# Kernel tuning notes

Hardware: AMD Instinct MI355X
Metric: run time of the kernel (lower is better)

## Reference

```python
import jax, jax.numpy as jnp
import numpy as np

B, NV, DM, DK, DV, H, DFF = 256, 40, 512, 256, 256, 4, 2048
K1, K2 = 4, 8
EPS = 1e-5


def _knn_mask(vertices, k):
    # square_distance(xyz, xyz): dist[b,i,j] = ||x_i - x_j||^2
    d = -2.0 * jnp.einsum('bic,bjc->bij', vertices, vertices)
    sq = jnp.sum(vertices ** 2, -1)
    d = d + sq[:, :, None] + sq[:, None, :]
    # torch.topk(dist, k, dim=1, largest=False)[1].transpose(1,2) -> [B,N,k]
    idx = jax.lax.top_k(-jnp.swapaxes(d, 1, 2), k)[1]
    counts = jax.nn.one_hot(idx, NV, dtype=jnp.float32).sum(-2)  # [B,N,NV]
    return (counts < 1.0)[:, None, :, :]  # [B,1,N,N], broadcasts over heads (== repeat)


def _ln(x, g, b):
    m = x.mean(-1, keepdims=True)
    v = x.var(-1, keepdims=True)
    return (x - m) / jnp.sqrt(v + EPS) * g + b


def _encoder(x, mask, wq, bq, wk, bk, wv, bv, wo, bo, ln1g, ln1b, w1, b1, w2, b2, ln2g, ln2b):
    Bn, N, _ = x.shape
    q = (x @ wq + bq).reshape(Bn, N, H, DK).transpose(0, 2, 1, 3)   # [B,H,N,DK]
    kk = (x @ wk + bk).reshape(Bn, N, H, DK).transpose(0, 2, 3, 1)  # [B,H,DK,N]
    v = (x @ wv + bv).reshape(Bn, N, H, DV).transpose(0, 2, 1, 3)   # [B,H,N,DV]
    att = jnp.matmul(q, kk) / np.sqrt(DK)                           # [B,H,N,N]
    att = jnp.where(mask, -jnp.inf, att)
    att = jax.nn.softmax(att, axis=-1)
    o = jnp.matmul(att, v).transpose(0, 2, 1, 3).reshape(Bn, N, H * DV) @ wo + bo
    x = _ln(x + o, ln1g, ln1b)                                      # residual + LayerNorm
    ff = jax.nn.relu(x @ w1 + b1) @ w2 + b2                         # position-wise FFN
    return _ln(x + ff, ln2g, ln2b)


def _fusion(y, w1, b1, bng, bnb, w2, b2):
    y = y @ w1 + b1                       # Conv1d(1024,512,1) == per-position linear
    m = y.mean((0, 1))
    v = y.var((0, 1))                     # BatchNorm1d, training-mode batch stats (biased var)
    y = (y - m) / jnp.sqrt(v + EPS) * bng + bnb
    y = jnp.where(y > 0, y, 0.2 * y)      # LeakyReLU(0.2)
    return y @ w2 + b2                    # Conv1d(512,512,1)


def _forward(vertices, F, *p):
    m1 = _knn_mask(vertices, K1)
    m2 = _knn_mask(vertices, K2)
    F1 = _encoder(F, m1, *p[0:16])
    F2 = _encoder(F, m2, *p[16:32])
    yy = jnp.concatenate((F1, F2), -1)    # [B,N,2*DM]
    return _fusion(yy, *p[32:38])


def setup_inputs() -> dict:
    key = jax.random.key(0)
    d = {}
    cnt = [0]
    def nk():
        cnt[0] += 1
        return jax.random.fold_in(key, cnt[0])
    def lin(i, o):
        return jax.random.normal(nk(), (i, o), jnp.float32) * (1.0 / np.sqrt(i))
    d['vertices'] = jax.random.normal(nk(), (B, NV, 3), jnp.float32)
    d['F'] = jax.random.normal(nk(), (B, NV, DM), jnp.float32)
    for pfx in ('e1', 'e2'):
        d[pfx + '_wq'] = lin(DM, H * DK); d[pfx + '_bq'] = jnp.zeros((H * DK,), jnp.float32)
        d[pfx + '_wk'] = lin(DM, H * DK); d[pfx + '_bk'] = jnp.zeros((H * DK,), jnp.float32)
        d[pfx + '_wv'] = lin(DM, H * DV); d[pfx + '_bv'] = jnp.zeros((H * DV,), jnp.float32)
        d[pfx + '_wo'] = lin(H * DV, DM); d[pfx + '_bo'] = jnp.zeros((DM,), jnp.float32)
        d[pfx + '_ln1g'] = jnp.ones((DM,), jnp.float32); d[pfx + '_ln1b'] = jnp.zeros((DM,), jnp.float32)
        d[pfx + '_w1'] = lin(DM, DFF); d[pfx + '_b1'] = jnp.zeros((DFF,), jnp.float32)
        d[pfx + '_w2'] = lin(DFF, DM); d[pfx + '_b2'] = jnp.zeros((DM,), jnp.float32)
        d[pfx + '_ln2g'] = jnp.ones((DM,), jnp.float32); d[pfx + '_ln2b'] = jnp.zeros((DM,), jnp.float32)
    d['fus_w1'] = lin(2 * DM, DM); d['fus_b1'] = jnp.zeros((DM,), jnp.float32)
    d['fus_bng'] = jnp.ones((DM,), jnp.float32); d['fus_bnb'] = jnp.zeros((DM,), jnp.float32)
    d['fus_w2'] = lin(DM, DM); d['fus_b2'] = jnp.zeros((DM,), jnp.float32)
    return d


def reference(vertices, F,
              e1_wq, e1_bq, e1_wk, e1_bk, e1_wv, e1_bv, e1_wo, e1_bo,
              e1_ln1g, e1_ln1b, e1_w1, e1_b1, e1_w2, e1_b2, e1_ln2g, e1_ln2b,
              e2_wq, e2_bq, e2_wk, e2_bk, e2_wv, e2_bv, e2_wo, e2_bo,
              e2_ln1g, e2_ln1b, e2_w1, e2_b1, e2_w2, e2_b2, e2_ln2g, e2_ln2b,
              fus_w1, fus_b1, fus_bng, fus_bnb, fus_w2, fus_b2):
    return _forward(vertices, F,
                    e1_wq, e1_bq, e1_wk, e1_bk, e1_wv, e1_bv, e1_wo, e1_bo,
                    e1_ln1g, e1_ln1b, e1_w1, e1_b1, e1_w2, e1_b2, e1_ln2g, e1_ln2b,
                    e2_wq, e2_bq, e2_wk, e2_bk, e2_wv, e2_bv, e2_wo, e2_bo,
                    e2_ln1g, e2_ln1b, e2_w1, e2_b1, e2_w2, e2_b2, e2_ln2g, e2_ln2b,
                    fus_w1, fus_b1, fus_bng, fus_bnb, fus_w2, fus_b2)
```

## Files before the change

kernel.cpp:

```cpp
#include <hip/hip_runtime.h>

typedef unsigned short u16;
typedef unsigned int   u32;
typedef __attribute__((ext_vector_type(4))) float f32x4;
typedef __attribute__((ext_vector_type(8))) short short8;
typedef __attribute__((ext_vector_type(4))) unsigned short u16x4;

#define DEV __device__ __forceinline__
#define AS1 __attribute__((address_space(1)))
#define AS3 __attribute__((address_space(3)))
#define SB  __builtin_amdgcn_sched_barrier(0)
#define BAR __builtin_amdgcn_s_barrier()

DEV float bf2f(u16 u){ return __uint_as_float(((u32)u)<<16); }
DEV u16 f2bf(float f){ u32 u=__float_as_uint(f); return (u16)((u + 0x7fffu + ((u>>16)&1u))>>16); }
DEV void g2lds16(const void* g, void* l){
  __builtin_amdgcn_global_load_lds((const AS1 void*)g, (AS3 void*)l, 16, 0, 0);
}

struct WtJobs {
  const float* W[14];
  u16*         WT[14];
  int K[14];
  int N[14];
  int off[15];
};

__global__ __launch_bounds__(256) void wtb_kernel(WtJobs J){
  __shared__ u16 tile[32][33];
  int bid = blockIdx.x;
  int j = 0;
  #pragma unroll
  for (int s=1;s<14;++s) if (bid >= J.off[s]) j = s;
  int lb = bid - J.off[j];
  int K = J.K[j], N = J.N[j];
  int nx = N>>5;
  int n0 = (lb % nx)<<5, k0 = (lb / nx)<<5;
  const float* W = J.W[j];
  u16* WT = J.WT[j];
  int tx = threadIdx.x, ty = threadIdx.y;
  #pragma unroll
  for (int i=0;i<4;++i){
    int k = ty + i*8;
    tile[k][tx] = f2bf(W[(size_t)(k0+k)*N + n0 + tx]);
  }
  __syncthreads();
  #pragma unroll
  for (int i=0;i<4;++i){
    int n = ty + i*8;
    WT[(size_t)(n0+n)*K + k0 + tx] = tile[tx][n];
  }
}

__global__ __launch_bounds__(256) void cvt_kernel(const float* __restrict__ in,
                                                  u16* __restrict__ out, long n4){
  long i = ((long)blockIdx.x*256 + threadIdx.x);
  if (i < n4){
    f32x4 v = *(const f32x4*)(in + i*4);
    u16x4 r; r.x=f2bf(v.x); r.y=f2bf(v.y); r.z=f2bf(v.z); r.w=f2bf(v.w);
    *(u16x4*)(out + i*4) = r;
  }
}

__global__ __launch_bounds__(256) void catb_kernel(const float* __restrict__ a,
                                                   const float* __restrict__ b,
                                                   const float* __restrict__ c,
                                                   float* __restrict__ dst){
  int i = blockIdx.x*256 + threadIdx.x;
  if (i < 1024) dst[i] = a[i];
  else if (i < 2048) dst[i] = b[i-1024];
  else if (i < 3072) dst[i] = c[i-2048];
}

__global__ __launch_bounds__(256) void fill_kernel(float* p, float v, long n){
  long i = (long)blockIdx.x*256 + threadIdx.x;
  if (i < n) p[i] = v;
}

__global__ __launch_bounds__(256) void knn_kernel(const float* __restrict__ verts,
                                                  unsigned char* __restrict__ nbr1,
                                                  unsigned char* __restrict__ nbr2){
  __shared__ float P[40][3];
  __shared__ float SQ[40];
  int b = blockIdx.x, tid = threadIdx.x, wave = tid>>6, lane = tid&63;
  if (tid < 40){
    float x = verts[((size_t)b*40+tid)*3+0];
    float y = verts[((size_t)b*40+tid)*3+1];
    float z = verts[((size_t)b*40+tid)*3+2];
    P[tid][0]=x; P[tid][1]=y; P[tid][2]=z;
    SQ[tid] = __fadd_rn(__fadd_rn(__fmul_rn(x,x),__fmul_rn(y,y)),__fmul_rn(z,z));
  }
  __syncthreads();
  for (int i = wave; i < 40; i += 4){
    float d = 3.0e38f;
    if (lane < 40){
      int j = lane;
      float dot = __fadd_rn(__fadd_rn(__fmul_rn(P[i][0],P[j][0]),
                                      __fmul_rn(P[i][1],P[j][1])),
                            __fmul_rn(P[i][2],P[j][2]));
      d = __fadd_rn(__fadd_rn(__fmul_rn(-2.f,dot), SQ[j]), SQ[i]);
    }
    bool taken = false;
    #pragma unroll
    for (int s=0;s<8;++s){
      float v = taken ? 3.0e38f : d;
      float m = v;
      #pragma unroll
      for (int o=32;o;o>>=1) m = fminf(m, __shfl_xor(m, o));
      unsigned long long mask = __ballot(v == m);
      int bj = __ffsll((unsigned long long)mask) - 1;
      if (lane == bj) taken = true;
      if (lane == 0){
        if (s < 4) nbr1[((size_t)b*40+i)*4+s] = (unsigned char)bj;
        nbr2[((size_t)b*40+i)*8+s] = (unsigned char)bj;
      }
    }
  }
}

struct GemmZ { const u16* A; const u16* BT; const float* bias; void* C; };

template<int RELU, int OUTBF>
__global__ __launch_bounds__(256, 4) void gemm_btz(GemmZ g0, GemmZ g1,
                                                   int M, int N, int K, int lda, int ldc){
  GemmZ g = blockIdx.z ? g1 : g0;
  __shared__ u16 As[128*32];
  __shared__ u16 Bs[128*32];
  const int tid  = threadIdx.x;
  const int wave = tid>>6, lane = tid&63;
  const int wr = (wave>>1)<<6, wc = (wave&1)<<6;
  const int row0 = blockIdx.x<<7, col0 = blockIdx.y<<7;
  f32x4 acc[4][4];
  #pragma unroll
  for (int i=0;i<4;++i)
    #pragma unroll
    for (int j=0;j<4;++j) acc[i][j] = (f32x4){0.f,0.f,0.f,0.f};

  const int rL = lane>>2;
  const int ch = lane&3;
  const int fr = lane&15, fc = lane>>4;
  const short8* Asv = (const short8*)As;
  const short8* Bsv = (const short8*)Bs;

  for (int kt=0; kt<K; kt+=32){
    #pragma unroll
    for (int c=0;c<2;++c){
      int lo = c*4096 + wave*1024;
      int r  = c*64 + wave*16 + rL;
      int kk = ((ch ^ ((r>>1)&3))<<3);
      g2lds16(g.A  + (size_t)(row0+r)*lda + kt + kk, (char*)As + lo);
      g2lds16(g.BT + (size_t)(col0+r)*K   + kt + kk, (char*)Bs + lo);
    }
    __syncthreads();
    short8 a[4], b[4];
    #pragma unroll
    for (int i=0;i<4;++i){
      int rowA = wr + i*16 + fr;
      int rowB = wc + i*16 + fr;
      a[i] = Asv[rowA*4 + (fc ^ ((rowA>>1)&3))];
      b[i] = Bsv[rowB*4 + (fc ^ ((rowB>>1)&3))];
    }
    #pragma unroll
    for (int i=0;i<4;++i)
      #pragma unroll
      for (int j=0;j<4;++j)
        acc[i][j] = __builtin_amdgcn_mfma_f32_16x16x32_bf16(a[i], b[j], acc[i][j], 0,0,0);
    __syncthreads();
  }
  #pragma unroll
  for (int i=0;i<4;++i){
    int mrow = row0 + wr + i*16 + fc*4;
    #pragma unroll
    for (int j=0;j<4;++j){
      int ncol = col0 + wc + j*16 + fr;
      float bv = g.bias[ncol];
      #pragma unroll
      for (int r=0;r<4;++r){
        float v = acc[i][j][r] + bv;
        if (RELU) v = v > 0.f ? v : 0.f;
        if (OUTBF) ((u16*)g.C)[(size_t)(mrow+r)*ldc + ncol] = f2bf(v);
        else       ((float*)g.C)[(size_t)(mrow+r)*ldc + ncol] = v;
      }
    }
  }
}

DEV void stage32(const u16* __restrict__ gbase, int ldg, u16* __restrict__ buf,
                 int kt, int wave, int lane){
  int srw = wave*16 + (lane>>2);
  int scl = (lane&3) ^ ((srw>>1)&3);
  const u16* src = gbase + (size_t)srw*ldg + kt + scl*8;
  char* dst = (char*)buf + wave*1024;
  g2lds16(src, dst);
  g2lds16(src + (size_t)128*ldg, dst + 8192);
}

template<int RELU>
__global__ __launch_bounds__(512, 1) void gemm256pz(GemmZ g0, GemmZ g1,
                                                    int M, int N, int K, int lda, int ldc){
  GemmZ g = blockIdx.z ? g1 : g0;
  __shared__ u16 As[4][256*32];
  __shared__ u16 Bs[4][256*32];
  const int tid  = threadIdx.x;
  const int wave = tid>>6, lane = tid&63;
  const int wm = wave>>2, wn = wave&3;
  const int fr = lane&15, fc = lane>>4;
  const int row0 = blockIdx.x<<8, col0 = blockIdx.y<<8;
  const int NT = K>>5;
  const u16* Ag = g.A  + (size_t)row0*lda;
  const u16* Bg = g.BT + (size_t)col0*K;

  f32x4 acc[8][4];
  #pragma unroll
  for (int i=0;i<8;++i)
    #pragma unroll
    for (int j=0;j<4;++j) acc[i][j] = (f32x4){0.f,0.f,0.f,0.f};

  stage32(Ag, lda, As[0], 0,  wave, lane);  stage32(Bg, K, Bs[0], 0,  wave, lane);
  stage32(Ag, lda, As[1], 32, wave, lane);  stage32(Bg, K, Bs[1], 32, wave, lane);
  stage32(Ag, lda, As[2], 64, wave, lane);  stage32(Bg, K, Bs[2], 64, wave, lane);
  asm volatile("s_waitcnt vmcnt(8)" ::: "memory");
  SB; BAR; SB;

  for (int t = 0; t < NT; ++t){
    const int cur = t&3, nx3 = (t+3)&3;
    const short8* AV = (const short8*)As[cur];
    const short8* BV = (const short8*)Bs[cur];
    short8 a[4], b[4];
    #pragma unroll
    for (int nf=0;nf<4;++nf){ int rr = wn*64 + nf*16 + fr; b[nf] = BV[rr*4 + (fc ^ ((rr>>1)&3))]; }
    #pragma unroll
    for (int mf=0;mf<4;++mf){ int rr = wm*128 + mf*16 + fr; a[mf] = AV[rr*4 + (fc ^ ((rr>>1)&3))]; }
    if (t+3 < NT) stage32(Ag, lda, As[nx3], (t+3)<<5, wave, lane);
    SB; BAR; SB;
    __builtin_amdgcn_s_setprio(1);
    #pragma unroll
    for (int mf=0;mf<4;++mf)
      #pragma unroll
      for (int nf=0;nf<4;++nf)
        acc[mf][nf] = __builtin_amdgcn_mfma_f32_16x16x32_bf16(a[mf], b[nf], acc[mf][nf], 0,0,0);
    __builtin_amdgcn_s_setprio(0);
    SB; BAR; SB;
    #pragma unroll
    for (int mf=0;mf<4;++mf){ int rr = wm*128 + (mf+4)*16 + fr; a[mf] = AV[rr*4 + (fc ^ ((rr>>1)&3))]; }
    if (t+3 < NT) stage32(Bg, K, Bs[nx3], (t+3)<<5, wave, lane);
    {
      int rem = NT - t - 1;
      if (rem >= 3)      asm volatile("s_waitcnt vmcnt(8)" ::: "memory");
      else if (rem == 2) asm volatile("s_waitcnt vmcnt(4)" ::: "memory");
      else if (rem == 1) asm volatile("s_waitcnt vmcnt(0)" ::: "memory");
    }
    SB; BAR; SB;
    __builtin_amdgcn_s_setprio(1);
    #pragma unroll
    for (int mf=0;mf<4;++mf)
      #pragma unroll
      for (int nf=0;nf<4;++nf)
        acc[mf+4][nf] = __builtin_amdgcn_mfma_f32_16x16x32_bf16(a[mf], b[nf], acc[mf+4][nf], 0,0,0);
    __builtin_amdgcn_s_setprio(0);
    SB; BAR; SB;
  }

  #pragma unroll
  for (int i=0;i<8;++i){
    int mrow = row0 + wm*128 + i*16 + fc*4;
    #pragma unroll
    for (int j=0;j<4;++j){
      int ncol = col0 + wn*64 + j*16 + fr;
      float bv = g.bias[ncol];
      #pragma unroll
      for (int r=0;r<4;++r){
        float v = acc[i][j][r] + bv;
        if (RELU) v = v > 0.f ? v : 0.f;
        ((u16*)g.C)[(size_t)(mrow+r)*ldc + ncol] = f2bf(v);
      }
    }
  }
}

template<int KNB>
__global__ __launch_bounds__(256) void attn_kernel(const u16* __restrict__ QKV,
                                                   const unsigned char* __restrict__ nbr,
                                                   u16* __restrict__ O, int ldo){
  __shared__ u16 KV[2][40*256];
  int b = blockIdx.x>>2, h = blockIdx.x&3;
  int tid = threadIdx.x, wave = tid>>6, lane = tid&63;
  const size_t rowb = (size_t)b*40;
  for (int c = tid; c < 1280; c += 256){
    int row = c >> 5, col = (c & 31) << 3;
    size_t src = (rowb+row)*3072 + h*256 + col;
    *(short8*)&KV[0][row*256+col] = *(const short8*)(QKV + src + 1024);
    *(short8*)&KV[1][row*256+col] = *(const short8*)(QKV + src + 2048);
  }
  __syncthreads();
  for (int i = wave; i < 40; i += 4){
    int js[KNB];
    if (KNB == 4){
      u32 p = *(const u32*)(nbr + (rowb+i)*4);
      js[0]=p&255; js[1]=(p>>8)&255; js[2]=(p>>16)&255; js[3]=(p>>24)&255;
    } else {
      u32 p0 = *(const u32*)(nbr + (rowb+i)*8);
      u32 p1 = *(const u32*)(nbr + (rowb+i)*8 + 4);
      js[0]=p0&255; js[1]=(p0>>8)&255; js[2]=(p0>>16)&255; js[3]=(p0>>24)&255;
      js[4]=p1&255; js[5]=(p1>>8)&255; js[6]=(p1>>16)&255; js[7]=(p1>>24)&255;
    }
    u16x4 qv = *(const u16x4*)(QKV + (rowb+i)*3072 + h*256 + lane*4);
    float q0=bf2f(qv.x), q1=bf2f(qv.y), q2=bf2f(qv.z), q3=bf2f(qv.w);
    float s[KNB];
    #pragma unroll
    for (int jj=0;jj<KNB;++jj){
      u16x4 kv = *(const u16x4*)&KV[0][js[jj]*256 + lane*4];
      s[jj] = q0*bf2f(kv.x) + q1*bf2f(kv.y) + q2*bf2f(kv.z) + q3*bf2f(kv.w);
    }
    #pragma unroll
    for (int jj=0;jj<KNB;++jj){
      #pragma unroll
      for (int o=32;o;o>>=1) s[jj] += __shfl_xor(s[jj], o);
      s[jj] *= 0.0625f;
    }
    float m = s[0];
    #pragma unroll
    for (int jj=1;jj<KNB;++jj) m = fmaxf(m, s[jj]);
    float sum = 0.f;
    #pragma unroll
    for (int jj=0;jj<KNB;++jj){ s[jj] = expf(s[jj]-m); sum += s[jj]; }
    float inv = 1.f/sum;
    float o0=0.f,o1=0.f,o2=0.f,o3=0.f;
    #pragma unroll
    for (int jj=0;jj<KNB;++jj){
      float w = s[jj]*inv;
      u16x4 vv = *(const u16x4*)&KV[1][js[jj]*256 + lane*4];
      o0 += w*bf2f(vv.x); o1 += w*bf2f(vv.y); o2 += w*bf2f(vv.z); o3 += w*bf2f(vv.w);
    }
    u16x4 r; r.x=f2bf(o0); r.y=f2bf(o1); r.z=f2bf(o2); r.w=f2bf(o3);
    *(u16x4*)(O + (rowb+i)*(size_t)ldo + h*256 + lane*4) = r;
  }
}

struct LnJob { const float* resf; const u16* delta; const float* g; const float* be;
               u16* outb; float* outf; };

DEV float blockReduce(float v, float* red){
  #pragma unroll
  for (int o=32;o;o>>=1) v += __shfl_xor(v, o);
  int lane = threadIdx.x&63, w = threadIdx.x>>6;
  if (lane==0) red[w] = v;
  __syncthreads();
  float t = red[0]+red[1]+red[2]+red[3];
  __syncthreads();
  return t;
}

__global__ __launch_bounds__(256) void ln2_kernel(LnJob j0, LnJob j1, int rstride){
  __shared__ float red[4];
  LnJob j = blockIdx.y ? j1 : j0;
  int row = blockIdx.x, tid = threadIdx.x;
  size_t ibr = (size_t)row*rstride + tid*2;
  size_t ibd = (size_t)row*1024 + tid*2;
  float2 xr = *(const float2*)(j.resf+ibr);
  u32 dp = *(const u32*)(j.delta+ibd);
  float x0 = xr.x + bf2f((u16)(dp&0xffffu));
  float x1 = xr.y + bf2f((u16)(dp>>16));
  float s = blockReduce(x0+x1, red);
  float mean = s*(1.f/512.f);
  float d0 = x0-mean, d1 = x1-mean;
  float q = blockReduce(d0*d0+d1*d1, red);
  float inv = 1.f/sqrtf(q*(1.f/512.f)+1e-5f);
  float2 gg = *(const float2*)(j.g+tid*2);
  float2 bb = *(const float2*)(j.be+tid*2);
  float r0 = d0*inv*gg.x + bb.x;
  float r1 = d1*inv*gg.y + bb.y;
  *(u32*)(j.outb + ibd) = ((u32)f2bf(r1)<<16) | (u32)f2bf(r0);
  if (j.outf) *(float2*)(j.outf + ibd) = make_float2(r0,r1);
}

__global__ __launch_bounds__(512) void bn_part(const float* __restrict__ y,
                                               float* __restrict__ psum, float* __restrict__ psq){
  int c = threadIdx.x, blk = blockIdx.x;
  float s = 0.f, q = 0.f;
  for (int r = blk; r < 10240; r += 256){
    float v = y[(size_t)r*512 + c];
    s += v; q += v*v;
  }
  psum[blk*512+c] = s; psq[blk*512+c] = q;
}

__global__ __launch_bounds__(512) void bn_fin(const float* __restrict__ psum,
                                              const float* __restrict__ psq,
                                              const float* __restrict__ g,
                                              const float* __restrict__ b,
                                              float* __restrict__ scale, float* __restrict__ shift){
  int c = threadIdx.x;
  float s = 0.f, q = 0.f;
  for (int k=0;k<256;++k){ s += psum[k*512+c]; q += psq[k*512+c]; }
  float m = s*(1.f/10240.f);
  float var = q*(1.f/10240.f) - m*m;
  float sc = g[c]/sqrtf(var + 1e-5f);
  scale[c] = sc; shift[c] = b[c] - m*sc;
}

__global__ __launch_bounds__(256) void bn_apply(const float* __restrict__ y,
                                                const float* __restrict__ scale,
                                                const float* __restrict__ shift,
                                                u16* __restrict__ out){
  long i4 = ((long)blockIdx.x*256 + threadIdx.x)*4;
  if (i4 < (long)10240*512){
    int c = (int)(i4 & 511);
    f32x4 v  = *(const f32x4*)(y+i4);
    f32x4 sc = *(const f32x4*)(scale+c);
    f32x4 sh = *(const f32x4*)(shift+c);
    f32x4 r;
    #pragma unroll
    for (int k=0;k<4;++k){
      float t = v[k]*sc[k] + sh[k];
      r[k] = t > 0.f ? t : 0.2f*t;
    }
    u16x4 o; o.x=f2bf(r[0]); o.y=f2bf(r[1]); o.z=f2bf(r[2]); o.w=f2bf(r[3]);
    *(u16x4*)(out+i4) = o;
  }
}

extern "C" void kernel_launch(void* const* d_in, const int* in_sizes, int n_in,
                              void* d_out, int out_size, void* d_ws, size_t ws_size,
                              hipStream_t stream){
  const float* verts = (const float*)d_in[0];
  const float* F     = (const float*)d_in[1];
  const float* ew[2][16];
  for (int e=0;e<2;++e) for (int i=0;i<16;++i) ew[e][i] = (const float*)d_in[2+e*16+i];
  const float* fus_w1  = (const float*)d_in[34];
  const float* fus_b1  = (const float*)d_in[35];
  const float* fus_bng = (const float*)d_in[36];
  const float* fus_bnb = (const float*)d_in[37];
  const float* fus_w2  = (const float*)d_in[38];
  const float* fus_b2  = (const float*)d_in[39];

  const int M = 10240;
  size_t off = 0;
  auto alloc = [&](size_t bytes)->void*{
    void* p = (char*)d_ws + off; off = (off + bytes + 255) & ~(size_t)255; return p;
  };
  u16 *wtqkv[2],*wto[2],*wtw1[2],*wtw2[2];
  float* bqkv[2];
  for (int e=0;e<2;++e){
    wtqkv[e] = (u16*)alloc((size_t)3072*512*2);
    wto[e]   = (u16*)alloc((size_t)512*1024*2);
    wtw1[e]  = (u16*)alloc((size_t)2048*512*2);
    wtw2[e]  = (u16*)alloc((size_t)512*2048*2);
    bqkv[e]  = (float*)alloc(3072*4);
  }
  u16*  wtf1 = (u16*)alloc((size_t)512*1024*2);
  u16*  wtf2 = (u16*)alloc((size_t)512*512*2);
  u16*  Fb   = (u16*)alloc((size_t)M*512*2);
  u16*  QKVb = (u16*)alloc((size_t)M*3072*2);
  u16*  H1   = (u16*)alloc((size_t)M*4096*2);
  u16*  PF   = (u16*)alloc((size_t)M*1024*2);
  u16*  X1b  = (u16*)alloc((size_t)M*1024*2);
  u16*  YC   = (u16*)alloc((size_t)M*1024*2);
  unsigned char* nbr1 = (unsigned char*)alloc(256*40*4);
  unsigned char* nbr2 = (unsigned char*)alloc(256*40*8);
  float* psum = (float*)alloc(256*512*4);
  float* psq  = (float*)alloc(256*512*4);
  float* bnsc = (float*)alloc(512*4);
  float* bnsh = (float*)alloc(512*4);
  u16*   OB  = H1;
  float* X1f = (float*)QKVb;
  float* Y1  = (float*)QKVb;
  u16*   Y2  = (u16*)((char*)QKVb + (size_t)24*1024*1024);

  if (off > ws_size){
    long n = out_size;
    fill_kernel<<<(unsigned)((n+255)/256),256,0,stream>>>((float*)d_out, 12345.0f, n);
    return;
  }

  WtJobs J;
  int nb = 0, ji = 0;
  auto addjob = [&](const float* W, u16* WT, int K, int N){
    J.W[ji]=W; J.WT[ji]=WT; J.K[ji]=K; J.N[ji]=N; J.off[ji]=nb;
    nb += (N>>5)*(K>>5); ++ji;
  };
  for (int e=0;e<2;++e){
    addjob(ew[e][0],  wtqkv[e],                    512, 1024);
    addjob(ew[e][2],  wtqkv[e]+(size_t)1024*512,   512, 1024);
    addjob(ew[e][4],  wtqkv[e]+(size_t)2048*512,   512, 1024);
    addjob(ew[e][6],  wto[e],  1024, 512);
    addjob(ew[e][10], wtw1[e], 512, 2048);
    addjob(ew[e][12], wtw2[e], 2048, 512);
  }
  addjob(fus_w1, wtf1, 1024, 512);
  addjob(fus_w2, wtf2, 512, 512);
  J.off[14] = nb;
  wtb_kernel<<<nb, dim3(32,8), 0, stream>>>(J);
  for (int e=0;e<2;++e)
    catb_kernel<<<12,256,0,stream>>>(ew[e][1], ew[e][3], ew[e][5], bqkv[e]);
  cvt_kernel<<<5120,256,0,stream>>>(F, Fb, (long)M*512/4);
  knn_kernel<<<256,256,0,stream>>>(verts, nbr1, nbr2);

  for (int e=0;e<2;++e){
    GemmZ q{Fb, wtqkv[e], bqkv[e], QKVb};
    gemm256pz<0><<<dim3(40,12,1),512,0,stream>>>(q, q, M, 3072, 512, 512, 3072);
    if (e == 0) attn_kernel<4><<<1024,256,0,stream>>>(QKVb, nbr1, OB,        2048);
    else        attn_kernel<8><<<1024,256,0,stream>>>(QKVb, nbr2, OB + 1024, 2048);
  }

  {
    GemmZ o0{OB,        wto[0], ew[0][7], PF};
    GemmZ o1{OB + 1024, wto[1], ew[1][7], PF + 512};
    gemm_btz<0,1><<<dim3(80,4,2),256,0,stream>>>(o0, o1, M, 512, 1024, 2048, 1024);
  }
  {
    LnJob a{F, PF,       ew[0][8], ew[0][9], X1b,       X1f};
    LnJob b{F, PF + 512, ew[1][8], ew[1][9], X1b + 512, X1f + 512};
    ln2_kernel<<<dim3(M,2),256,0,stream>>>(a, b, 512);
  }
  {
    GemmZ f0{X1b,       wtw1[0], ew[0][11], H1};
    GemmZ f1{X1b + 512, wtw1[1], ew[1][11], H1 + 2048};
    gemm256pz<1><<<dim3(40,8,2),512,0,stream>>>(f0, f1, M, 2048, 512, 1024, 4096);
  }
  {
    GemmZ f0{H1,        wtw2[0], ew[0][13], PF};
    GemmZ f1{H1 + 2048, wtw2[1], ew[1][13], PF + 512};
    gemm_btz<0,1><<<dim3(80,4,2),256,0,stream>>>(f0, f1, M, 512, 2048, 4096, 1024);
  }
  {
    LnJob a{X1f,       PF,       ew[0][14], ew[0][15], YC,       nullptr};
    LnJob b{X1f + 512, PF + 512, ew[1][14], ew[1][15], YC + 512, nullptr};
    ln2_kernel<<<dim3(M,2),256,0,stream>>>(a, b, 1024);
  }

  {
    GemmZ fz{YC, wtf1, fus_b1, Y1};
    gemm_btz<0,0><<<dim3(80,4,1),256,0,stream>>>(fz, fz, M, 512, 1024, 1024, 512);
  }
  bn_part<<<256,512,0,stream>>>(Y1, psum, psq);
  bn_fin<<<1,512,0,stream>>>(psum, psq, fus_bng, fus_bnb, bnsc, bnsh);
  bn_apply<<<5120,256,0,stream>>>(Y1, bnsc, bnsh, Y2);
  {
    GemmZ fz{Y2, wtf2, fus_b2, d_out};
    gemm_btz<0,0><<<dim3(80,4,1),256,0,stream>>>(fz, fz, M, 512, 512, 512, 512);
  }
}
```

Baseline: 461.4 us.

## Merge prep kernels into one launch and batch both encoders' QKV and attention

Four preprocessing kernels become one prep_kernel that picks its role from the block index: weight transpose to bf16, QKV bias concatenation, F conversion and the kNN search. Both encoders' QKV projections now run as a single z=2 GEMM launch. Encoder 2 writes its QKV into a second buffer aliased onto PF (and, past its end, the following X1b/YC space). The two attention passes are likewise merged into one z=2 launch. This is meant to cut launch overhead and serialization and to give the GPU more concurrent blocks, at the cost of relying on those buffers being laid out contiguously.

Result: slower. 473.5 us (+2.6%).

```diff
diff --git a/kernel.cpp b/kernel.cpp
--- a/kernel.cpp
+++ b/kernel.cpp
@@ -25,97 +25,97 @@
   int N[14];
   int off[15];
 };
-
-__global__ __launch_bounds__(256) void wtb_kernel(WtJobs J){
-  __shared__ u16 tile[32][33];
-  int bid = blockIdx.x;
-  int j = 0;
-  #pragma unroll
-  for (int s=1;s<14;++s) if (bid >= J.off[s]) j = s;
-  int lb = bid - J.off[j];
-  int K = J.K[j], N = J.N[j];
-  int nx = N>>5;
-  int n0 = (lb % nx)<<5, k0 = (lb / nx)<<5;
-  const float* W = J.W[j];
-  u16* WT = J.WT[j];
-  int tx = threadIdx.x, ty = threadIdx.y;
-  #pragma unroll
-  for (int i=0;i<4;++i){
-    int k = ty + i*8;
-    tile[k][tx] = f2bf(W[(size_t)(k0+k)*N + n0 + tx]);
-  }
-  __syncthreads();
-  #pragma unroll
-  for (int i=0;i<4;++i){
-    int n = ty + i*8;
-    WT[(size_t)(n0+n)*K + k0 + tx] = tile[tx][n];
-  }
-}
-
-__global__ __launch_bounds__(256) void cvt_kernel(const float* __restrict__ in,
-                                                  u16* __restrict__ out, long n4){
-  long i = ((long)blockIdx.x*256 + threadIdx.x);
-  if (i < n4){
-    f32x4 v = *(const f32x4*)(in + i*4);
-    u16x4 r; r.x=f2bf(v.x); r.y=f2bf(v.y); r.z=f2bf(v.z); r.w=f2bf(v.w);
-    *(u16x4*)(out + i*4) = r;
-  }
-}
-
-__global__ __launch_bounds__(256) void catb_kernel(const float* __restrict__ a,
-                                                   const float* __restrict__ b,
-                                                   const float* __restrict__ c,
-                                                   float* __restrict__ dst){
-  int i = blockIdx.x*256 + threadIdx.x;
-  if (i < 1024) dst[i] = a[i];
-  else if (i < 2048) dst[i] = b[i-1024];
-  else if (i < 3072) dst[i] = c[i-2048];
+struct PrepArgs {
+  WtJobs J;
+  const float* qb[2][3];
+  float*       bq[2];
+  const float* F; u16* Fb; long n4;
+  const float* verts; unsigned char* nbr1; unsigned char* nbr2;
+};
+
+__global__ __launch_bounds__(256) void prep_kernel(PrepArgs P){
+  int bid = blockIdx.x, tid = threadIdx.x;
+  int nwt = P.J.off[14];
+  if (bid < nwt){
+    __shared__ u16 tile[32][33];
+    int j = 0;
+    #pragma unroll
+    for (int s=1;s<14;++s) if (bid >= P.J.off[s]) j = s;
+    int lb = bid - P.J.off[j];
+    int K = P.J.K[j], N = P.J.N[j];
+    int nx = N>>5;
+    int n0 = (lb % nx)<<5, k0 = (lb / nx)<<5;
+    const float* W = P.J.W[j];
+    u16* WT = P.J.WT[j];
+    int tx = tid&31, ty = tid>>5;
+    #pragma unroll
+    for (int i=0;i<4;++i){
+      int k = ty + i*8;
+      tile[k][tx] = f2bf(W[(size_t)(k0+k)*N + n0 + tx]);
+    }
+    __syncthreads();
+    #pragma unroll
+    for (int i=0;i<4;++i){
+      int n = ty + i*8;
+      WT[(size_t)(n0+n)*K + k0 + tx] = tile[tx][n];
+    }
+  } else if (bid < nwt + 24){
+    int lb = bid - nwt;
+    int e = lb / 12;
+    int i = (lb % 12)*256 + tid;
+    float v = (i < 1024) ? P.qb[e][0][i] : (i < 2048) ? P.qb[e][1][i-1024] : P.qb[e][2][i-2048];
+    P.bq[e][i] = v;
+  } else if (bid < nwt + 24 + 5120){
+    long i = ((long)(bid - nwt - 24)*256 + tid);
+    if (i < P.n4){
+      f32x4 v = *(const f32x4*)(P.F + i*4);
+      u16x4 r; r.x=f2bf(v.x); r.y=f2bf(v.y); r.z=f2bf(v.z); r.w=f2bf(v.w);
+      *(u16x4*)(P.Fb + i*4) = r;
+    }
+  } else {
+    __shared__ float Pv[40][3];
+    __shared__ float SQ[40];
+    int b = bid - nwt - 24 - 5120;
+    int wave = tid>>6, lane = tid&63;
+    if (tid < 40){
+      float x = P.verts[((size_t)b*40+tid)*3+0];
+      float y = P.verts[((size_t)b*40+tid)*3+1];
+      float z = P.verts[((size_t)b*40+tid)*3+2];
+      Pv[tid][0]=x; Pv[tid][1]=y; Pv[tid][2]=z;
+      SQ[tid] = __fadd_rn(__fadd_rn(__fmul_rn(x,x),__fmul_rn(y,y)),__fmul_rn(z,z));
+    }
+    __syncthreads();
+    for (int i = wave; i < 40; i += 4){
+      float d = 3.0e38f;
+      if (lane < 40){
+        int j = lane;
+        float dot = __fadd_rn(__fadd_rn(__fmul_rn(Pv[i][0],Pv[j][0]),
+                                        __fmul_rn(Pv[i][1],Pv[j][1])),
+                              __fmul_rn(Pv[i][2],Pv[j][2]));
+        d = __fadd_rn(__fadd_rn(__fmul_rn(-2.f,dot), SQ[j]), SQ[i]);
+      }
+      bool taken = false;
+      #pragma unroll
+      for (int s=0;s<8;++s){
+        float v = taken ? 3.0e38f : d;
+        float m = v;
+        #pragma unroll
+        for (int o=32;o;o>>=1) m = fminf(m, __shfl_xor(m, o));
+        unsigned long long mask = __ballot(v == m);
+        int bj = __ffsll((unsigned long long)mask) - 1;
+        if (lane == bj) taken = true;
+        if (lane == 0){
+          if (s < 4) P.nbr1[((size_t)b*40+i)*4+s] = (unsigned char)bj;
+          P.nbr2[((size_t)b*40+i)*8+s] = (unsigned char)bj;
+        }
+      }
+    }
+  }
 }
 
 __global__ __launch_bounds__(256) void fill_kernel(float* p, float v, long n){
   long i = (long)blockIdx.x*256 + threadIdx.x;
   if (i < n) p[i] = v;
-}
-
-__global__ __launch_bounds__(256) void knn_kernel(const float* __restrict__ verts,
-                                                  unsigned char* __restrict__ nbr1,
-                                                  unsigned char* __restrict__ nbr2){
-  __shared__ float P[40][3];
-  __shared__ float SQ[40];
-  int b = blockIdx.x, tid = threadIdx.x, wave = tid>>6, lane = tid&63;
-  if (tid < 40){
-    float x = verts[((size_t)b*40+tid)*3+0];
-    float y = verts[((size_t)b*40+tid)*3+1];
-    float z = verts[((size_t)b*40+tid)*3+2];
-    P[tid][0]=x; P[tid][1]=y; P[tid][2]=z;
-    SQ[tid] = __fadd_rn(__fadd_rn(__fmul_rn(x,x),__fmul_rn(y,y)),__fmul_rn(z,z));
-  }
-  __syncthreads();
-  for (int i = wave; i < 40; i += 4){
-    float d = 3.0e38f;
-    if (lane < 40){
-      int j = lane;
-      float dot = __fadd_rn(__fadd_rn(__fmul_rn(P[i][0],P[j][0]),
-                                      __fmul_rn(P[i][1],P[j][1])),
-                            __fmul_rn(P[i][2],P[j][2]));
-      d = __fadd_rn(__fadd_rn(__fmul_rn(-2.f,dot), SQ[j]), SQ[i]);
-    }
-    bool taken = false;
-    #pragma unroll
-    for (int s=0;s<8;++s){
-      float v = taken ? 3.0e38f : d;
-      float m = v;
-      #pragma unroll
-      for (int o=32;o;o>>=1) m = fminf(m, __shfl_xor(m, o));
-      unsigned long long mask = __ballot(v == m);
-      int bj = __ffsll((unsigned long long)mask) - 1;
-      if (lane == bj) taken = true;
-      if (lane == 0){
-        if (s < 4) nbr1[((size_t)b*40+i)*4+s] = (unsigned char)bj;
-        nbr2[((size_t)b*40+i)*8+s] = (unsigned char)bj;
-      }
-    }
-  }
 }
 
 struct GemmZ { const u16* A; const u16* BT; const float* bias; void* C; };
@@ -278,11 +278,11 @@
   }
 }
 
+struct AttnZ { const u16* QKV; const unsigned char* nbr; u16* O; };
+
 template<int KNB>
-__global__ __launch_bounds__(256) void attn_kernel(const u16* __restrict__ QKV,
-                                                   const unsigned char* __restrict__ nbr,
-                                                   u16* __restrict__ O, int ldo){
-  __shared__ u16 KV[2][40*256];
+DEV void attn_body(const u16* __restrict__ QKV, const unsigned char* __restrict__ nbr,
+                   u16* __restrict__ O, u16 KV[2][40*256]){
   int b = blockIdx.x>>2, h = blockIdx.x&3;
   int tid = threadIdx.x, wave = tid>>6, lane = tid&63;
   const size_t rowb = (size_t)b*40;
@@ -333,8 +333,14 @@
       o0 += w*bf2f(vv.x); o1 += w*bf2f(vv.y); o2 += w*bf2f(vv.z); o3 += w*bf2f(vv.w);
     }
     u16x4 r; r.x=f2bf(o0); r.y=f2bf(o1); r.z=f2bf(o2); r.w=f2bf(o3);
-    *(u16x4*)(O + (rowb+i)*(size_t)ldo + h*256 + lane*4) = r;
-  }
+    *(u16x4*)(O + (rowb+i)*2048 + h*256 + lane*4) = r;
+  }
+}
+
+__global__ __launch_bounds__(256) void attn2_kernel(AttnZ a0, AttnZ a1){
+  __shared__ u16 KV[2][40*256];
+  if (blockIdx.z == 0) attn_body<4>(a0.QKV, a0.nbr, a0.O, KV);
+  else                 attn_body<8>(a1.QKV, a1.nbr, a1.O, KV);
 }
 
 struct LnJob { const float* resf; const u16* delta; const float* g; const float* be;
@@ -462,6 +468,7 @@
   float* psq  = (float*)alloc(256*512*4);
   float* bnsc = (float*)alloc(512*4);
   float* bnsh = (float*)alloc(512*4);
+  u16*   QKV2 = PF;
   u16*   OB  = H1;
   float* X1f = (float*)QKVb;
   float* Y1  = (float*)QKVb;
@@ -473,10 +480,10 @@
     return;
   }
 
-  WtJobs J;
+  PrepArgs P;
   int nb = 0, ji = 0;
   auto addjob = [&](const float* W, u16* WT, int K, int N){
-    J.W[ji]=W; J.WT[ji]=WT; J.K[ji]=K; J.N[ji]=N; J.off[ji]=nb;
+    P.J.W[ji]=W; P.J.WT[ji]=WT; P.J.K[ji]=K; P.J.N[ji]=N; P.J.off[ji]=nb;
     nb += (N>>5)*(K>>5); ++ji;
   };
   for (int e=0;e<2;++e){
@@ -489,18 +496,23 @@
   }
   addjob(fus_w1, wtf1, 1024, 512);
   addjob(fus_w2, wtf2, 512, 512);
-  J.off[14] = nb;
-  wtb_kernel<<<nb, dim3(32,8), 0, stream>>>(J);
-  for (int e=0;e<2;++e)
-    catb_kernel<<<12,256,0,stream>>>(ew[e][1], ew[e][3], ew[e][5], bqkv[e]);
-  cvt_kernel<<<5120,256,0,stream>>>(F, Fb, (long)M*512/4);
-  knn_kernel<<<256,256,0,stream>>>(verts, nbr1, nbr2);
-
+  P.J.off[14] = nb;
   for (int e=0;e<2;++e){
-    GemmZ q{Fb, wtqkv[e], bqkv[e], QKVb};
-    gemm256pz<0><<<dim3(40,12,1),512,0,stream>>>(q, q, M, 3072, 512, 512, 3072);
-    if (e == 0) attn_kernel<4><<<1024,256,0,stream>>>(QKVb, nbr1, OB,        2048);
-    else        attn_kernel<8><<<1024,256,0,stream>>>(QKVb, nbr2, OB + 1024, 2048);
+    P.qb[e][0]=ew[e][1]; P.qb[e][1]=ew[e][3]; P.qb[e][2]=ew[e][5]; P.bq[e]=bqkv[e];
+  }
+  P.F = F; P.Fb = Fb; P.n4 = (long)M*512/4;
+  P.verts = verts; P.nbr1 = nbr1; P.nbr2 = nbr2;
+  prep_kernel<<<nb + 24 + 5120 + 256, 256, 0, stream>>>(P);
+
+  {
+    GemmZ q0{Fb, wtqkv[0], bqkv[0], QKVb};
+    GemmZ q1{Fb, wtqkv[1], bqkv[1], QKV2};
+    gemm256pz<0><<<dim3(40,12,2),512,0,stream>>>(q0, q1, M, 3072, 512, 512, 3072);
+  }
+  {
+    AttnZ a0{QKVb, nbr1, OB};
+    AttnZ a1{QKV2, nbr2, OB + 1024};
+    attn2_kernel<<<dim3(1024,1,2),256,0,stream>>>(a0, a1);
   }
 
   {
```

## Batch QKV GEMMs for both encoders and keep intermediates in bf16

Applied to the files above, without the earlier changes.

Both encoders' QKV projections now run in one launch using a second buffer, followed by the two attention kernels. The bias-concat kernels merge into one launch. The LN1 output is no longer written as fp32; LN2 reads the bf16 residual instead. The fusion conv1 output is stored as bf16 rather than fp32, which halves the traffic for the BN statistics and apply passes. This cuts launches and memory traffic at the cost of extra rounding in the residual path and the batch-norm input.

Result: faster. 450.4 us (median of 2 runs) (-2.4%).

```diff
diff --git a/kernel.cpp b/kernel.cpp
--- a/kernel.cpp
+++ b/kernel.cpp
@@ -62,14 +62,15 @@
   }
 }
 
-__global__ __launch_bounds__(256) void catb_kernel(const float* __restrict__ a,
-                                                   const float* __restrict__ b,
-                                                   const float* __restrict__ c,
-                                                   float* __restrict__ dst){
-  int i = blockIdx.x*256 + threadIdx.x;
-  if (i < 1024) dst[i] = a[i];
-  else if (i < 2048) dst[i] = b[i-1024];
-  else if (i < 3072) dst[i] = c[i-2048];
+__global__ __launch_bounds__(256) void catb2_kernel(const float* a0, const float* b0, const float* c0, float* d0,
+                                                    const float* a1, const float* b1, const float* c1, float* d1){
+  int lb = blockIdx.x;
+  int e = lb / 12;
+  int i = (lb % 12)*256 + threadIdx.x;
+  const float* a = e ? a1 : a0;  const float* b = e ? b1 : b0;
+  const float* c = e ? c1 : c0;  float* d = e ? d1 : d0;
+  float v = (i < 1024) ? a[i] : (i < 2048) ? b[i-1024] : c[i-2048];
+  d[i] = v;
 }
 
 __global__ __launch_bounds__(256) void fill_kernel(float* p, float v, long n){
@@ -337,8 +338,7 @@
   }
 }
 
-struct LnJob { const float* resf; const u16* delta; const float* g; const float* be;
-               u16* outb; float* outf; };
+struct LnJob { const void* resf; const u16* delta; const float* g; const float* be; u16* outb; };
 
 DEV float blockReduce(float v, float* red){
   #pragma unroll
@@ -351,16 +351,23 @@
   return t;
 }
 
+template<int RBF>
 __global__ __launch_bounds__(256) void ln2_kernel(LnJob j0, LnJob j1, int rstride){
   __shared__ float red[4];
   LnJob j = blockIdx.y ? j1 : j0;
   int row = blockIdx.x, tid = threadIdx.x;
-  size_t ibr = (size_t)row*rstride + tid*2;
   size_t ibd = (size_t)row*1024 + tid*2;
-  float2 xr = *(const float2*)(j.resf+ibr);
+  float x0, x1;
+  if (RBF){
+    u32 rp = *(const u32*)((const u16*)j.resf + (size_t)row*rstride + tid*2);
+    x0 = bf2f((u16)(rp&0xffffu)); x1 = bf2f((u16)(rp>>16));
+  } else {
+    float2 xr = *(const float2*)((const float*)j.resf + (size_t)row*rstride + tid*2);
+    x0 = xr.x; x1 = xr.y;
+  }
   u32 dp = *(const u32*)(j.delta+ibd);
-  float x0 = xr.x + bf2f((u16)(dp&0xffffu));
-  float x1 = xr.y + bf2f((u16)(dp>>16));
+  x0 += bf2f((u16)(dp&0xffffu));
+  x1 += bf2f((u16)(dp>>16));
   float s = blockReduce(x0+x1, red);
   float mean = s*(1.f/512.f);
   float d0 = x0-mean, d1 = x1-mean;
@@ -371,15 +378,14 @@
   float r0 = d0*inv*gg.x + bb.x;
   float r1 = d1*inv*gg.y + bb.y;
   *(u32*)(j.outb + ibd) = ((u32)f2bf(r1)<<16) | (u32)f2bf(r0);
-  if (j.outf) *(float2*)(j.outf + ibd) = make_float2(r0,r1);
-}
-
-__global__ __launch_bounds__(512) void bn_part(const float* __restrict__ y,
+}
+
+__global__ __launch_bounds__(512) void bn_part(const u16* __restrict__ y,
                                                float* __restrict__ psum, float* __restrict__ psq){
   int c = threadIdx.x, blk = blockIdx.x;
   float s = 0.f, q = 0.f;
   for (int r = blk; r < 10240; r += 256){
-    float v = y[(size_t)r*512 + c];
+    float v = bf2f(y[(size_t)r*512 + c]);
     s += v; q += v*v;
   }
   psum[blk*512+c] = s; psq[blk*512+c] = q;
@@ -399,23 +405,24 @@
   scale[c] = sc; shift[c] = b[c] - m*sc;
 }
 
-__global__ __launch_bounds__(256) void bn_apply(const float* __restrict__ y,
+__global__ __launch_bounds__(256) void bn_apply(const u16* __restrict__ y,
                                                 const float* __restrict__ scale,
                                                 const float* __restrict__ shift,
                                                 u16* __restrict__ out){
   long i4 = ((long)blockIdx.x*256 + threadIdx.x)*4;
   if (i4 < (long)10240*512){
     int c = (int)(i4 & 511);
-    f32x4 v  = *(const f32x4*)(y+i4);
+    u16x4 v4 = *(const u16x4*)(y+i4);
     f32x4 sc = *(const f32x4*)(scale+c);
     f32x4 sh = *(const f32x4*)(shift+c);
-    f32x4 r;
+    float vv[4] = {bf2f(v4.x), bf2f(v4.y), bf2f(v4.z), bf2f(v4.w)};
+    u16x4 o;
     #pragma unroll
     for (int k=0;k<4;++k){
-      float t = v[k]*sc[k] + sh[k];
-      r[k] = t > 0.f ? t : 0.2f*t;
-    }
-    u16x4 o; o.x=f2bf(r[0]); o.y=f2bf(r[1]); o.z=f2bf(r[2]); o.w=f2bf(r[3]);
+      float t = vv[k]*sc[k] + sh[k];
+      t = t > 0.f ? t : 0.2f*t;
+      ((u16*)&o)[k] = f2bf(t);
+    }
     *(u16x4*)(out+i4) = o;
   }
 }
@@ -462,10 +469,10 @@
   float* psq  = (float*)alloc(256*512*4);
   float* bnsc = (float*)alloc(512*4);
   float* bnsh = (float*)alloc(512*4);
+  u16*   QKV2 = PF;
   u16*   OB  = H1;
-  float* X1f = (float*)QKVb;
-  float* Y1  = (float*)QKVb;
-  u16*   Y2  = (u16*)((char*)QKVb + (size_t)24*1024*1024);
+  u16*   Y1b = (u16*)QKVb;
+  u16*   Y2  = (u16*)((char*)QKVb + (size_t)12*1024*1024);
 
   if (off > ws_size){
     long n = out_size;
@@ -491,17 +498,18 @@
   addjob(fus_w2, wtf2, 512, 512);
   J.off[14] = nb;
   wtb_kernel<<<nb, dim3(32,8), 0, stream>>>(J);
-  for (int e=0;e<2;++e)
-    catb_kernel<<<12,256,0,stream>>>(ew[e][1], ew[e][3], ew[e][5], bqkv[e]);
+  catb2_kernel<<<24,256,0,stream>>>(ew[0][1], ew[0][3], ew[0][5], bqkv[0],
+                                    ew[1][1], ew[1][3], ew[1][5], bqkv[1]);
   cvt_kernel<<<5120,256,0,stream>>>(F, Fb, (long)M*512/4);
   knn_kernel<<<256,256,0,stream>>>(verts, nbr1, nbr2);
 
-  for (int e=0;e<2;++e){
-    GemmZ q{Fb, wtqkv[e], bqkv[e], QKVb};
-    gemm256pz<0><<<dim3(40,12,1),512,0,stream>>>(q, q, M, 3072, 512, 512, 3072);
-    if (e == 0) attn_kernel<4><<<1024,256,0,stream>>>(QKVb, nbr1, OB,        2048);
-    else        attn_kernel<8><<<1024,256,0,stream>>>(QKVb, nbr2, OB + 1024, 2048);
-  }
+  {
+    GemmZ q0{Fb, wtqkv[0], bqkv[0], QKVb};
+    GemmZ q1{Fb, wtqkv[1], bqkv[1], QKV2};
+    gemm256pz<0><<<dim3(40,12,2),512,0,stream>>>(q0, q1, M, 3072, 512, 512, 3072);
+  }
+  attn_kernel<4><<<1024,256,0,stream>>>(QKVb, nbr1, OB,        2048);
+  attn_kernel<8><<<1024,256,0,stream>>>(QKV2, nbr2, OB + 1024, 2048);
 
   {
     GemmZ o0{OB,        wto[0], ew[0][7], PF};
@@ -509,9 +517,9 @@
     gemm_btz<0,1><<<dim3(80,4,2),256,0,stream>>>(o0, o1, M, 512, 1024, 2048, 1024);
   }
   {
-    LnJob a{F, PF,       ew[0][8], ew[0][9], X1b,       X1f};
-    LnJob b{F, PF + 512, ew[1][8], ew[1][9], X1b + 512, X1f + 512};
-    ln2_kernel<<<dim3(M,2),256,0,stream>>>(a, b, 512);
+    LnJob a{F, PF,       ew[0][8], ew[0][9], X1b};
+    LnJob b{F, PF + 512, ew[1][8], ew[1][9], X1b + 512};
+    ln2_kernel<0><<<dim3(M,2),256,0,stream>>>(a, b, 512);
   }
   {
     GemmZ f0{X1b,       wtw1[0], ew[0][11], H1};
@@ -524,18 +532,18 @@
     gemm_btz<0,1><<<dim3(80,4,2),256,0,stream>>>(f0, f1, M, 512, 2048, 4096, 1024);
   }
   {
-    LnJob a{X1f,       PF,       ew[0][14], ew[0][15], YC,       nullptr};
-    LnJob b{X1f + 512, PF + 512, ew[1][14], ew[1][15], YC + 512, nullptr};
-    ln2_kernel<<<dim3(M,2),256,0,stream>>>(a, b, 1024);
-  }
-
-  {
-    GemmZ fz{YC, wtf1, fus_b1, Y1};
-    gemm_btz<0,0><<<dim3(80,4,1),256,0,stream>>>(fz, fz, M, 512, 1024, 1024, 512);
-  }
-  bn_part<<<256,512,0,stream>>>(Y1, psum, psq);
+    LnJob a{X1b,       PF,       ew[0][14], ew[0][15], YC};
+    LnJob b{X1b + 512, PF + 512, ew[1][14], ew[1][15], YC + 512};
+    ln2_kernel<1><<<dim3(M,2),256,0,stream>>>(a, b, 1024);
+  }
+
+  {
+    GemmZ fz{YC, wtf1, fus_b1, Y1b};
+    gemm_btz<0,1><<<dim3(80,4,1),256,0,stream>>>(fz, fz, M, 512, 1024, 1024, 512);
+  }
+  bn_part<<<256,512,0,stream>>>(Y1b, psum, psq);
   bn_fin<<<1,512,0,stream>>>(psum, psq, fus_bng, fus_bnb, bnsc, bnsh);
-  bn_apply<<<5120,256,0,stream>>>(Y1, bnsc, bnsh, Y2);
+  bn_apply<<<5120,256,0,stream>>>(Y1b, bnsc, bnsh, Y2);
   {
     GemmZ fz{Y2, wtf2, fus_b2, d_out};
     gemm_btz<0,0><<<dim3(80,4,1),256,0,stream>>>(fz, fz, M, 512, 512, 512, 512);
```
